# Performance work log

Hardware: AMD Instinct MI355X
Metric: run time of the kernel (lower is better)

The kernel has to match this reference:

```python
import jax, jax.numpy as jnp
import numpy as np

N = 50000
E = 800000
IN_C = 128
HID = 256
OUT_C = 40


def setup_inputs() -> dict:
    key = jax.random.key(0)
    ks = jax.random.split(key, 12)
    def glorot(k, shape):
        lim = float(np.sqrt(6.0 / (shape[0] + shape[1])))
        return jax.random.uniform(k, shape, jnp.float32, -lim, lim)
    x = jax.random.normal(ks[0], (N, IN_C), jnp.float32)
    edge_index = jax.random.randint(ks[1], (2, E), 0, N, jnp.int64)
    edge_weight = jax.random.uniform(ks[2], (E,), jnp.float32)
    return {
        "x": x,
        "edge_index": edge_index,
        "edge_weight": edge_weight,
        "w1_rel": glorot(ks[3], (IN_C, HID)),
        "b1": jnp.zeros((HID,), jnp.float32),
        "w1_root": glorot(ks[4], (IN_C, HID)),
        "w2_rel": glorot(ks[5], (HID, HID)),
        "b2": jnp.zeros((HID,), jnp.float32),
        "w2_root": glorot(ks[6], (HID, HID)),
        "w_lin": glorot(ks[7], (2 * HID, OUT_C)),
        "b_lin": jnp.zeros((OUT_C,), jnp.float32),
    }


def graph_conv(x, src, dst, w, w_rel, b_rel, w_root):
    # PyG GraphConv (aggr='add'): lin_rel(scatter_add(x[src]*w)) + lin_root(x)
    msg = x[src] * w[:, None]                      # [E, F]
    agg = jax.ops.segment_sum(msg, dst, num_segments=N)  # [N, F]
    return agg @ w_rel + b_rel + x @ w_root


def reference(x, edge_index, edge_weight, w1_rel, b1, w1_root,
              w2_rel, b2, w2_root, w_lin, b_lin):
    src, dst = edge_index[0], edge_index[1]
    x1 = jax.nn.relu(graph_conv(x, src, dst, edge_weight, w1_rel, b1, w1_root))
    # dropout is a no-op in eval mode
    x2 = jax.nn.relu(graph_conv(x1, src, dst, edge_weight, w2_rel, b2, w2_root))
    h = jnp.concatenate([x1, x2], axis=-1)         # [N, 2*HID]
    logits = h @ w_lin + b_lin                     # [N, OUT_C]
    return jax.nn.log_softmax(logits, axis=-1)
```

## Files before the change

### kernel.cpp

```cpp
#include <hip/hip_runtime.h>
#include <hip/hip_bf16.h>
#include <hip/hip_fp16.h>
#include <math.h>


typedef __attribute__((ext_vector_type(8))) short short8;
typedef __attribute__((ext_vector_type(4))) float f32x4;

static __device__ __forceinline__ float bf2f(unsigned short u) {
    return __uint_as_float(((unsigned)u) << 16);
}

static __device__ __forceinline__ void fp8x4_to_f32(unsigned u, float* o) {
#if __has_builtin(__builtin_amdgcn_cvt_pk_f32_fp8)
    auto lo = __builtin_amdgcn_cvt_pk_f32_fp8((int)u, false);
    auto hi = __builtin_amdgcn_cvt_pk_f32_fp8((int)u, true);
    o[0] = lo[0]; o[1] = lo[1]; o[2] = hi[0]; o[3] = hi[1];
#else
#pragma unroll
    for (int i = 0; i < 4; ++i) {
        unsigned b = (u >> (8 * i)) & 0xffu;
        unsigned short hb = (unsigned short)(((b & 0x80u) << 8) | ((b & 0x7fu) << 7));
        o[i] = __half2float(__ushort_as_half(hb)) * 256.0f;
    }
#endif
}

static __device__ __forceinline__ unsigned f32_to_fp8(float f) {
    __half h = __float2half(f * 0.00390625f);
    unsigned short hb = __half_as_ushort(h);
    unsigned mag = hb & 0x7fffu;
    unsigned s = (hb >> 8) & 0x80u;
    unsigned v = (mag + 0x3fu + ((mag >> 7) & 1u)) >> 7;
    if (v > 0x7eu) v = 0x7eu;
    return s | v;
}

__global__ __launch_bounds__(256) void scan_block_sums(
    const int* __restrict__ counts, int* __restrict__ bsum, int n)
{
    __shared__ int sh[256];
    int idx = blockIdx.x * 256 + threadIdx.x;
    sh[threadIdx.x] = (idx < n) ? counts[idx] : 0;
    __syncthreads();
#pragma unroll
    for (int off = 128; off; off >>= 1) {
        if (threadIdx.x < off) sh[threadIdx.x] += sh[threadIdx.x + off];
        __syncthreads();
    }
    if (threadIdx.x == 0) bsum[blockIdx.x] = sh[0];
}

__global__ __launch_bounds__(256) void scan_bsum(
    const int* __restrict__ bsum, int* __restrict__ bpre,
    int* __restrict__ bucket_cursor, int nb)
{
    __shared__ int sh[256];
    int t = threadIdx.x;
    int v = (t < nb) ? bsum[t] : 0;
    sh[t] = v;
    __syncthreads();
#pragma unroll
    for (int off = 1; off < 256; off <<= 1) {
        int u = (t >= off) ? sh[t - off] : 0;
        __syncthreads();
        sh[t] += u;
        __syncthreads();
    }
    bpre[t]          = sh[t] - v;
    bucket_cursor[t] = sh[t] - v;
}

__global__ __launch_bounds__(256) void scan_final(
    const int* __restrict__ counts, const int* __restrict__ bpre,
    int* __restrict__ row_ptr, int n, int Etot)
{
    __shared__ int sh[256];
    int t = threadIdx.x;
    int idx = blockIdx.x * 256 + t;
    int v = (idx < n) ? counts[idx] : 0;
    sh[t] = v;
    __syncthreads();
#pragma unroll
    for (int off = 1; off < 256; off <<= 1) {
        int u = (t >= off) ? sh[t - off] : 0;
        __syncthreads();
        sh[t] += u;
        __syncthreads();
    }
    if (idx < n) row_ptr[idx] = bpre[blockIdx.x] + sh[t] - v;
    if (idx == 0) row_ptr[n] = Etot;
}

#define P1_EPB 8
__global__ __launch_bounds__(256) void part_kernel(
    const int* __restrict__ ei, const float* __restrict__ ew,
    int* __restrict__ bucket_cursor, uint2* __restrict__ part, int E)
{
    __shared__ int lhist[256];
    __shared__ int gbase[256];
    const int t = threadIdx.x;
    const int base = blockIdx.x * (256 * P1_EPB);
    lhist[t] = 0;
    __syncthreads();

    int pk[P1_EPB];
#pragma unroll
    for (int i = 0; i < P1_EPB; ++i) {
        int e = base + i * 256 + t;
        if (e < E) {
            int b = ei[E + e] >> 8;
            int r = atomicAdd(&lhist[b], 1);
            pk[i] = (b << 16) | r;
        } else pk[i] = -1;
    }
    __syncthreads();
    if (lhist[t] > 0) gbase[t] = atomicAdd(&bucket_cursor[t], lhist[t]);
    __syncthreads();
#pragma unroll
    for (int i = 0; i < P1_EPB; ++i) {
        if (pk[i] >= 0) {
            int e = base + i * 256 + t;
            int d = ei[E + e];
            unsigned short w16 = __half_as_ushort(__float2half(ew[e]));
            unsigned rec = ((unsigned)w16 << 16) | (unsigned)ei[e];
            int pos = gbase[pk[i] >> 16] + (pk[i] & 0xffff);
            part[pos] = make_uint2(rec, (unsigned)d);
        }
    }
}

__global__ __launch_bounds__(256) void fill2_kernel(
    const uint2* __restrict__ part, const int* __restrict__ bpre,
    const int* __restrict__ bsum, const int* __restrict__ row_ptr,
    unsigned* __restrict__ edges, int n)
{
    __shared__ int curs[256];
    const int b = blockIdx.x;
    const int t = threadIdx.x;
    const int node0 = b << 8;
    if (node0 + t < n) curs[t] = row_ptr[node0 + t];
    __syncthreads();
    const int beg = bpre[b];
    const int end = beg + bsum[b];
    for (int i = beg + t; i < end; i += 256) {
        uint2 p = part[i];
        int slot = atomicAdd(&curs[p.y & 255u], 1);
        edges[slot] = p.x;
    }
}

__global__ __launch_bounds__(256) void prep_all(
    const int* __restrict__ ei, int* __restrict__ counts, int E,
    const float* __restrict__ x, __hip_bfloat16* __restrict__ xb,
    unsigned char* __restrict__ xb8, int NX8,
    const float* __restrict__ w1_rel, const float* __restrict__ w1_root,
    const float* __restrict__ w2_rel, const float* __restrict__ w2_root,
    const float* __restrict__ w_lin,
    __hip_bfloat16* __restrict__ w1relT, __hip_bfloat16* __restrict__ w1rootT,
    __hip_bfloat16* __restrict__ w2relT, __hip_bfloat16* __restrict__ w2rootT,
    __hip_bfloat16* __restrict__ wlinT)
{
    int idx = blockIdx.x * 256 + threadIdx.x;
    if (idx < E) {
        atomicAdd(&counts[ei[E + idx]], 1);
        return;
    }
    idx -= E;
    if (idx < NX8) {
        float4 a = *(const float4*)&x[(size_t)idx * 8];
        float4 b = *(const float4*)&x[(size_t)idx * 8 + 4];
        float f[8] = { a.x, a.y, a.z, a.w, b.x, b.y, b.z, b.w };
        __hip_bfloat16 o[8];
#pragma unroll
        for (int i = 0; i < 8; ++i) o[i] = __float2bfloat16(f[i]);
        *(short8*)&xb[(size_t)idx * 8] = *(short8*)o;
        unsigned p0 = 0, p1 = 0;
#pragma unroll
        for (int i = 0; i < 4; ++i) p0 |= f32_to_fp8(f[i]) << (8 * i);
#pragma unroll
        for (int i = 0; i < 4; ++i) p1 |= f32_to_fp8(f[4 + i]) << (8 * i);
        *(uint2*)&xb8[(size_t)idx * 8] = make_uint2(p0, p1);
        return;
    }
    idx -= NX8;
    if (idx < 65536) {
        const float* src = (idx < 32768) ? w1_rel : w1_root;
        __hip_bfloat16* dst = (idx < 32768) ? w1relT : w1rootT;
        int i = idx & 32767;
        int k = i >> 8, c = i & 255;
        dst[c * 128 + k] = __float2bfloat16(src[i]);
    } else if (idx < 196608) {
        int j = idx - 65536;
        const float* src = (j < 65536) ? w2_rel : w2_root;
        __hip_bfloat16* dst = (j < 65536) ? w2relT : w2rootT;
        int i = j & 65535;
        int k = i >> 8, c = i & 255;
        dst[c * 256 + k] = __float2bfloat16(src[i]);
    } else if (idx < 229376) {
        int i = idx - 196608;
        int seg = i >> 14, c = (i >> 8) & 63, k = i & 255;
        float v = (c < 40) ? w_lin[(size_t)(seg * 256 + k) * 40 + c] : 0.f;
        wlinT[i] = __float2bfloat16(v);
    }
}

template <int C>
__global__ __launch_bounds__(256) void gather_fp8(
    const unsigned char* __restrict__ feat8,
    const unsigned* __restrict__ edges,
    const int*  __restrict__ rp,
    __hip_bfloat16* __restrict__ agg, int n)
{
    const int node = (blockIdx.x * 256 + threadIdx.x) >> 6;
    const int lane = threadIdx.x & 63;
    if (node >= n) return;
    const int beg = __builtin_amdgcn_readfirstlane(rp[node]);
    const int end = __builtin_amdgcn_readfirstlane(rp[node + 1]);

    constexpr int EPW = (C == 128) ? 8 : 4;
    constexpr int LPR = 64 / EPW;
    const int es = lane / LPR;
    const int ch = lane % LPR;
    const unsigned coff = (unsigned)ch * 16;

    float acc[16] = {};

    auto accum16 = [&](uint4 u, float w) {
        unsigned uu[4] = { u.x, u.y, u.z, u.w };
#pragma unroll
        for (int q = 0; q < 4; ++q) {
            float f[4];
            fp8x4_to_f32(uu[q], f);
#pragma unroll
            for (int i = 0; i < 4; ++i)
                acc[q * 4 + i] = fmaf(f[i], w, acc[q * 4 + i]);
        }
    };

    auto unpack_w = [](unsigned p) {
        return __half2float(__ushort_as_half((unsigned short)(p >> 16)));
    };

    for (int base = beg; base < end; base += 64) {
        const int m = min(64, end - base);
        unsigned ev = edges[base + ((lane < m) ? lane : (m - 1))];
        if (lane >= m) ev &= 0xffffu;

        int s = 0;
        for (; s + 2 * EPW <= m; s += 2 * EPW) {
            int j0 = s + es, j1 = j0 + EPW;
            unsigned p0 = (unsigned)__shfl((int)ev, j0, 64);
            unsigned p1 = (unsigned)__shfl((int)ev, j1, 64);
            uint4 u0 = *(const uint4*)(feat8 + (size_t)(p0 & 0xffffu) * C + coff);
            uint4 u1 = *(const uint4*)(feat8 + (size_t)(p1 & 0xffffu) * C + coff);
            accum16(u0, unpack_w(p0));
            accum16(u1, unpack_w(p1));
        }
        for (; s < m; s += EPW) {
            int j = min(s + es, 63);
            unsigned p = (unsigned)__shfl((int)ev, j, 64);
            uint4 u = *(const uint4*)(feat8 + (size_t)(p & 0xffffu) * C + coff);
            accum16(u, unpack_w(p));
        }
    }

#pragma unroll
    for (int k = 0; k < 16; ++k) {
        if constexpr (C == 128) {
            acc[k] += __shfl_xor(acc[k], 8, 64);
            acc[k] += __shfl_xor(acc[k], 16, 64);
            acc[k] += __shfl_xor(acc[k], 32, 64);
        } else {
            acc[k] += __shfl_xor(acc[k], 16, 64);
            acc[k] += __shfl_xor(acc[k], 32, 64);
        }
    }
    if (es == 0) {
        __hip_bfloat16 o[16];
#pragma unroll
        for (int k = 0; k < 16; ++k) o[k] = __float2bfloat16(acc[k]);
        __hip_bfloat16* op = agg + (size_t)node * C + ch * 16;
        *(short8*)op       = *(short8*)o;
        *(short8*)(op + 8) = *(short8*)(o + 8);
    }
}

template <bool WRITE_FP8>
__global__ __launch_bounds__(256) void gemm_mfma(
    const __hip_bfloat16* __restrict__ A0, const __hip_bfloat16* __restrict__ A1,
    const __hip_bfloat16* __restrict__ W0T, const __hip_bfloat16* __restrict__ W1T,
    const float* __restrict__ bias,
    __hip_bfloat16* __restrict__ Cmat,
    unsigned char* __restrict__ Cfp8,
    int n, int K0, int K1)
{
    __shared__ __hip_bfloat16 Asl[2][128 * 64];
    __shared__ __hip_bfloat16 Bsl[2][128 * 64];
    const int bm = blockIdx.x >> 1;
    const int bn = blockIdx.x & 1;
    const int row0 = bm * 128, col0 = bn * 128;
    const int t = threadIdx.x, lane = t & 63, wid = t >> 6;
    const int wr = wid >> 1, wc = wid & 1;

    const int S0 = K0 >> 6;
    const int S  = S0 + (K1 >> 6);

    auto stage = [&](int buf, int s) {
        const __hip_bfloat16* A;
        const __hip_bfloat16* WT;
        int K, k0;
        if (s < S0) { A = A0; WT = W0T; K = K0; k0 = s << 6; }
        else        { A = A1; WT = W1T; K = K1; k0 = (s - S0) << 6; }
#pragma unroll
        for (int i = 0; i < 4; ++i) {
            int idx = i * 256 + t;
            int r = idx >> 3, c = idx & 7;
            int gr = row0 + r; if (gr >= n) gr = n - 1;
            const __hip_bfloat16* srcA =
                A + (size_t)gr * K + k0 + ((c ^ (r & 7)) << 3);
            __builtin_amdgcn_global_load_lds(
                (const __attribute__((address_space(1))) void*)srcA,
                (__attribute__((address_space(3))) void*)&Asl[buf][idx * 8], 16, 0, 0);
            const __hip_bfloat16* srcB =
                WT + (size_t)(col0 + r) * K + k0 + ((c ^ (r & 7)) << 3);
            __builtin_amdgcn_global_load_lds(
                (const __attribute__((address_space(1))) void*)srcB,
                (__attribute__((address_space(3))) void*)&Bsl[buf][idx * 8], 16, 0, 0);
        }
    };

    f32x4 acc[4][4] = {};

    stage(0, 0);
    __syncthreads();

    for (int s = 0; s < S; ++s) {
        const int buf = s & 1;
        if (s + 1 < S) stage(buf ^ 1, s + 1);
#pragma unroll
        for (int kh = 0; kh < 2; ++kh) {
            const int cchunk = kh * 4 + (lane >> 4);
            short8 af[4], bfr[4];
#pragma unroll
            for (int m = 0; m < 4; ++m) {
                int r = wr * 64 + m * 16 + (lane & 15);
                af[m] = *(const short8*)&Asl[buf][r * 64 + ((cchunk ^ (r & 7)) << 3)];
            }
#pragma unroll
            for (int nn = 0; nn < 4; ++nn) {
                int r = wc * 64 + nn * 16 + (lane & 15);
                bfr[nn] = *(const short8*)&Bsl[buf][r * 64 + ((cchunk ^ (r & 7)) << 3)];
            }
#pragma unroll
            for (int m = 0; m < 4; ++m)
#pragma unroll
                for (int nn = 0; nn < 4; ++nn)
                    acc[m][nn] = __builtin_amdgcn_mfma_f32_16x16x32_bf16(
                        af[m], bfr[nn], acc[m][nn], 0, 0, 0);
        }
        __syncthreads();
    }

    __hip_bfloat16* Csh = &Asl[0][0];
#pragma unroll
    for (int nn = 0; nn < 4; ++nn) {
        int lcol = wc * 64 + nn * 16 + (lane & 15);
        float b = bias[col0 + lcol];
#pragma unroll
        for (int m = 0; m < 4; ++m) {
#pragma unroll
            for (int rg = 0; rg < 4; ++rg) {
                int lrow = wr * 64 + m * 16 + ((lane >> 4) * 4) + rg;
                float v = fmaxf(acc[m][nn][rg] + b, 0.f);
                Csh[lrow * 128 + lcol] = __float2bfloat16(v);
            }
        }
    }
    __syncthreads();

#pragma unroll
    for (int it = 0; it < 8; ++it) {
        int idx = it * 256 + t;
        int r = idx >> 4, c16 = idx & 15;
        if (row0 + r < n)
            *(short8*)(Cmat + (size_t)(row0 + r) * 256 + col0 + c16 * 8) =
                *(const short8*)&Csh[r * 128 + c16 * 8];
    }
    if constexpr (WRITE_FP8) {
#pragma unroll
        for (int it = 0; it < 4; ++it) {
            int idx = it * 256 + t;
            int r = idx >> 3, c16 = idx & 7;
            if (row0 + r < n) {
                const __hip_bfloat16* src = &Csh[r * 128 + c16 * 16];
                unsigned w[4];
#pragma unroll
                for (int q = 0; q < 4; ++q) {
                    unsigned p = 0;
#pragma unroll
                    for (int i = 0; i < 4; ++i)
                        p |= f32_to_fp8(__bfloat162float(src[q * 4 + i])) << (8 * i);
                    w[q] = p;
                }
                *(uint4*)(Cfp8 + (size_t)(row0 + r) * 256 + col0 + c16 * 16) =
                    make_uint4(w[0], w[1], w[2], w[3]);
            }
        }
    }
}

__global__ __launch_bounds__(256) void head_mfma(
    const __hip_bfloat16* __restrict__ X1, const __hip_bfloat16* __restrict__ X2,
    const __hip_bfloat16* __restrict__ WLT,
    const float* __restrict__ b_lin,
    float* __restrict__ out, int n)
{
    __shared__ __hip_bfloat16 Asl[128 * 64];
    __shared__ __hip_bfloat16 Bsl[64 * 64];
    const int row0 = blockIdx.x * 128;
    const int t = threadIdx.x, lane = t & 63, wid = t >> 6;

    f32x4 acc[2][4] = {};

    for (int seg = 0; seg < 2; ++seg) {
        const __hip_bfloat16* A  = seg ? X2 : X1;
        const __hip_bfloat16* WT = WLT + seg * 64 * 256;
        for (int k0 = 0; k0 < 256; k0 += 64) {
#pragma unroll
            for (int i = 0; i < 4; ++i) {
                int idx = i * 256 + t;
                int r = idx >> 3, c = idx & 7;
                int gr = row0 + r; if (gr >= n) gr = n - 1;
                const __hip_bfloat16* srcA =
                    A + (size_t)gr * 256 + k0 + ((c ^ (r & 7)) << 3);
                __builtin_amdgcn_global_load_lds(
                    (const __attribute__((address_space(1))) void*)srcA,
                    (__attribute__((address_space(3))) void*)&Asl[idx * 8], 16, 0, 0);
            }
#pragma unroll
            for (int i = 0; i < 2; ++i) {
                int idx = i * 256 + t;
                int r = idx >> 3, c = idx & 7;
                const __hip_bfloat16* srcB =
                    WT + (size_t)r * 256 + k0 + ((c ^ (r & 7)) << 3);
                __builtin_amdgcn_global_load_lds(
                    (const __attribute__((address_space(1))) void*)srcB,
                    (__attribute__((address_space(3))) void*)&Bsl[idx * 8], 16, 0, 0);
            }
            __syncthreads();
#pragma unroll
            for (int kh = 0; kh < 2; ++kh) {
                const int cchunk = kh * 4 + (lane >> 4);
                short8 af[2], bfr[4];
#pragma unroll
                for (int m = 0; m < 2; ++m) {
                    int r = wid * 32 + m * 16 + (lane & 15);
                    af[m] = *(const short8*)&Asl[r * 64 + ((cchunk ^ (r & 7)) << 3)];
                }
#pragma unroll
                for (int nn = 0; nn < 4; ++nn) {
                    int r = nn * 16 + (lane & 15);
                    bfr[nn] = *(const short8*)&Bsl[r * 64 + ((cchunk ^ (r & 7)) << 3)];
                }
#pragma unroll
                for (int m = 0; m < 2; ++m)
#pragma unroll
                    for (int nn = 0; nn < 4; ++nn)
                        acc[m][nn] = __builtin_amdgcn_mfma_f32_16x16x32_bf16(
                            af[m], bfr[nn], acc[m][nn], 0, 0, 0);
            }
            __syncthreads();
        }
    }

    const int cl = lane & 15;
    float bb[4];
#pragma unroll
    for (int nn = 0; nn < 4; ++nn) {
        int col = nn * 16 + cl;
        bb[nn] = (col < 40) ? b_lin[col] : 0.f;
    }
#pragma unroll
    for (int m = 0; m < 2; ++m) {
#pragma unroll
        for (int rg = 0; rg < 4; ++rg) {
            float v[4];
            float mx = -1e30f;
#pragma unroll
            for (int nn = 0; nn < 4; ++nn) {
                int col = nn * 16 + cl;
                v[nn] = acc[m][nn][rg] + bb[nn];
                if (col < 40) mx = fmaxf(mx, v[nn]);
            }
#pragma unroll
            for (int off = 1; off < 16; off <<= 1)
                mx = fmaxf(mx, __shfl_xor(mx, off, 64));
            float s = 0.f;
#pragma unroll
            for (int nn = 0; nn < 4; ++nn) {
                int col = nn * 16 + cl;
                if (col < 40) s += expf(v[nn] - mx);
            }
#pragma unroll
            for (int off = 1; off < 16; off <<= 1)
                s += __shfl_xor(s, off, 64);
            float ls = logf(s);
            int row = row0 + wid * 32 + m * 16 + ((lane >> 4) * 4) + rg;
            if (row < n) {
#pragma unroll
                for (int nn = 0; nn < 4; ++nn) {
                    int col = nn * 16 + cl;
                    if (col < 40)
                        out[(size_t)row * 40 + col] = v[nn] - mx - ls;
                }
            }
        }
    }
}

extern "C" void kernel_launch(void* const* d_in, const int* in_sizes, int n_in,
                              void* d_out, int out_size, void* d_ws, size_t ws_size,
                              hipStream_t stream)
{
    const float* x       = (const float*)d_in[0];
    const int*   ei      = (const int*)  d_in[1];
    const float* ew      = (const float*)d_in[2];
    const float* w1_rel  = (const float*)d_in[3];
    const float* b1      = (const float*)d_in[4];
    const float* w1_root = (const float*)d_in[5];
    const float* w2_rel  = (const float*)d_in[6];
    const float* b2      = (const float*)d_in[7];
    const float* w2_root = (const float*)d_in[8];
    const float* w_lin   = (const float*)d_in[9];
    const float* b_lin   = (const float*)d_in[10];
    float* out = (float*)d_out;

    const int N = in_sizes[0] / 128;
    const int E = in_sizes[2];

    auto align = [](char*& p, size_t bytes) {
        char* r = p;
        p += (bytes + 255) & ~(size_t)255;
        return r;
    };
    char* wp = (char*)d_ws;
    __hip_bfloat16* xb     = (__hip_bfloat16*)align(wp, (size_t)N * 128 * 2);
    __hip_bfloat16* agg1b  = (__hip_bfloat16*)align(wp, (size_t)N * 128 * 2);
    __hip_bfloat16* x1b    = (__hip_bfloat16*)align(wp, (size_t)N * 256 * 2);
    __hip_bfloat16* agg2b  = (__hip_bfloat16*)align(wp, (size_t)N * 256 * 2);
    __hip_bfloat16* x2b    = (__hip_bfloat16*)align(wp, (size_t)N * 256 * 2);
    unsigned char*  xb8    = (unsigned char*)align(wp, (size_t)N * 128);
    unsigned char*  x1b8   = (unsigned char*)align(wp, (size_t)N * 256);
    __hip_bfloat16* w1relT  = (__hip_bfloat16*)align(wp, 256 * 128 * 2);
    __hip_bfloat16* w1rootT = (__hip_bfloat16*)align(wp, 256 * 128 * 2);
    __hip_bfloat16* w2relT  = (__hip_bfloat16*)align(wp, 256 * 256 * 2);
    __hip_bfloat16* w2rootT = (__hip_bfloat16*)align(wp, 256 * 256 * 2);
    __hip_bfloat16* wlinT   = (__hip_bfloat16*)align(wp, 2 * 64 * 256 * 2);
    int*      counts        = (int*)align(wp, (size_t)N * 4);
    int*      row_ptr       = (int*)align(wp, (size_t)(N + 1) * 4);
    int*      bsum          = (int*)align(wp, 256 * 4);
    int*      bpre          = (int*)align(wp, 256 * 4);
    int*      bucket_cursor = (int*)align(wp, 256 * 4);
    unsigned* edges         = (unsigned*)align(wp, (size_t)E * 4);
    uint2*    part          = (uint2*)align(wp, (size_t)E * 8);

    const int eb = (E + 255) / 256;
    const int nb = (N + 255) / 256;

    hipMemsetAsync(counts, 0, (size_t)N * 4, stream);
    const int NX8 = N * 128 / 8;
    {
        long long total = (long long)E + NX8 + 229376;
        int blocks = (int)((total + 255) / 256);
        prep_all<<<blocks, 256, 0, stream>>>(
            ei, counts, E, x, xb, xb8, NX8,
            w1_rel, w1_root, w2_rel, w2_root, w_lin,
            w1relT, w1rootT, w2relT, w2rootT, wlinT);
    }
    scan_block_sums<<<nb, 256, 0, stream>>>(counts, bsum, N);
    scan_bsum<<<1, 256, 0, stream>>>(bsum, bpre, bucket_cursor, nb);
    scan_final<<<nb, 256, 0, stream>>>(counts, bpre, row_ptr, N, E);
    {
        int p1_blocks = (E + 256 * P1_EPB - 1) / (256 * P1_EPB);
        part_kernel<<<p1_blocks, 256, 0, stream>>>(ei, ew, bucket_cursor, part, E);
        fill2_kernel<<<nb, 256, 0, stream>>>(part, bpre, bsum, row_ptr, edges, N);
    }

    const int gather_blocks = (N * 64 + 255) / 256;
    const int gemm_grid     = ((N + 127) / 128) * 2;
    const int head_grid     = (N + 127) / 128;

    gather_fp8<128><<<gather_blocks, 256, 0, stream>>>(
        xb8, edges, row_ptr, agg1b, N);
    gemm_mfma<true><<<gemm_grid, 256, 0, stream>>>(
        agg1b, xb, w1relT, w1rootT, b1, x1b, x1b8, N, 128, 128);
    gather_fp8<256><<<gather_blocks, 256, 0, stream>>>(
        x1b8, edges, row_ptr, agg2b, N);
    gemm_mfma<false><<<gemm_grid, 256, 0, stream>>>(
        agg2b, x1b, w2relT, w2rootT, b2, x2b, nullptr, N, 256, 256);
    head_mfma<<<head_grid, 256, 0, stream>>>(x1b, x2b, wlinT, b_lin, out, N);
}
```

Before: 208.0 us.

## Replace per-node count and scans with bucket histogram and in-fill local scan

Removes the per-node global atomic degree counting, the block-sum scan and the final scan. Instead, a shared-memory bucket histogram over 256-node buckets is built, and fill2_kernel computes per-node counts and an exclusive scan locally from the partitioned edges, writing row_ptr itself. This cuts global atomics and two kernel launches, but fill2 now reads the partitioned edges twice.

Result: faster. 181.8 us (-12.6%).

```diff
diff --git a/kernel.cpp b/kernel.cpp
--- a/kernel.cpp
+++ b/kernel.cpp
@@ -36,28 +36,31 @@
     return s | v;
 }
 
-__global__ __launch_bounds__(256) void scan_block_sums(
-    const int* __restrict__ counts, int* __restrict__ bsum, int n)
-{
-    __shared__ int sh[256];
-    int idx = blockIdx.x * 256 + threadIdx.x;
-    sh[threadIdx.x] = (idx < n) ? counts[idx] : 0;
-    __syncthreads();
-#pragma unroll
-    for (int off = 128; off; off >>= 1) {
-        if (threadIdx.x < off) sh[threadIdx.x] += sh[threadIdx.x + off];
-        __syncthreads();
-    }
-    if (threadIdx.x == 0) bsum[blockIdx.x] = sh[0];
+#define BH_EPB 16
+__global__ __launch_bounds__(256) void bucket_hist(
+    const int* __restrict__ ei, int* __restrict__ bhist, int E)
+{
+    __shared__ int lh[256];
+    const int t = threadIdx.x;
+    lh[t] = 0;
+    __syncthreads();
+    const int base = blockIdx.x * (256 * BH_EPB);
+#pragma unroll
+    for (int i = 0; i < BH_EPB; ++i) {
+        int e = base + i * 256 + t;
+        if (e < E) atomicAdd(&lh[ei[E + e] >> 8], 1);
+    }
+    __syncthreads();
+    if (lh[t] > 0) atomicAdd(&bhist[t], lh[t]);
 }
 
 __global__ __launch_bounds__(256) void scan_bsum(
-    const int* __restrict__ bsum, int* __restrict__ bpre,
+    const int* __restrict__ bhist, int* __restrict__ bpre,
     int* __restrict__ bucket_cursor, int nb)
 {
     __shared__ int sh[256];
     int t = threadIdx.x;
-    int v = (t < nb) ? bsum[t] : 0;
+    int v = (t < nb) ? bhist[t] : 0;
     sh[t] = v;
     __syncthreads();
 #pragma unroll
@@ -69,27 +72,6 @@
     }
     bpre[t]          = sh[t] - v;
     bucket_cursor[t] = sh[t] - v;
-}
-
-__global__ __launch_bounds__(256) void scan_final(
-    const int* __restrict__ counts, const int* __restrict__ bpre,
-    int* __restrict__ row_ptr, int n, int Etot)
-{
-    __shared__ int sh[256];
-    int t = threadIdx.x;
-    int idx = blockIdx.x * 256 + t;
-    int v = (idx < n) ? counts[idx] : 0;
-    sh[t] = v;
-    __syncthreads();
-#pragma unroll
-    for (int off = 1; off < 256; off <<= 1) {
-        int u = (t >= off) ? sh[t - off] : 0;
-        __syncthreads();
-        sh[t] += u;
-        __syncthreads();
-    }
-    if (idx < n) row_ptr[idx] = bpre[blockIdx.x] + sh[t] - v;
-    if (idx == 0) row_ptr[n] = Etot;
 }
 
 #define P1_EPB 8
@@ -132,17 +114,37 @@
 
 __global__ __launch_bounds__(256) void fill2_kernel(
     const uint2* __restrict__ part, const int* __restrict__ bpre,
-    const int* __restrict__ bsum, const int* __restrict__ row_ptr,
+    const int* __restrict__ bhist, int* __restrict__ row_ptr,
     unsigned* __restrict__ edges, int n)
 {
+    __shared__ int lcnt[256];
+    __shared__ int excl[256];
     __shared__ int curs[256];
     const int b = blockIdx.x;
     const int t = threadIdx.x;
     const int node0 = b << 8;
-    if (node0 + t < n) curs[t] = row_ptr[node0 + t];
+    lcnt[t] = 0;
     __syncthreads();
     const int beg = bpre[b];
-    const int end = beg + bsum[b];
+    const int end = beg + bhist[b];
+    for (int i = beg + t; i < end; i += 256)
+        atomicAdd(&lcnt[part[i].y & 255u], 1);
+    __syncthreads();
+    int v = lcnt[t];
+    excl[t] = v;
+    __syncthreads();
+#pragma unroll
+    for (int off = 1; off < 256; off <<= 1) {
+        int u = (t >= off) ? excl[t - off] : 0;
+        __syncthreads();
+        excl[t] += u;
+        __syncthreads();
+    }
+    const int base_t = beg + excl[t] - v;
+    const int nd = node0 + t;
+    if (nd <= n) row_ptr[nd] = base_t;
+    curs[t] = base_t;
+    __syncthreads();
     for (int i = beg + t; i < end; i += 256) {
         uint2 p = part[i];
         int slot = atomicAdd(&curs[p.y & 255u], 1);
@@ -151,7 +153,6 @@
 }
 
 __global__ __launch_bounds__(256) void prep_all(
-    const int* __restrict__ ei, int* __restrict__ counts, int E,
     const float* __restrict__ x, __hip_bfloat16* __restrict__ xb,
     unsigned char* __restrict__ xb8, int NX8,
     const float* __restrict__ w1_rel, const float* __restrict__ w1_root,
@@ -162,11 +163,6 @@
     __hip_bfloat16* __restrict__ wlinT)
 {
     int idx = blockIdx.x * 256 + threadIdx.x;
-    if (idx < E) {
-        atomicAdd(&counts[ei[E + idx]], 1);
-        return;
-    }
-    idx -= E;
     if (idx < NX8) {
         float4 a = *(const float4*)&x[(size_t)idx * 8];
         float4 b = *(const float4*)&x[(size_t)idx * 8 + 4];
@@ -557,34 +553,32 @@
     __hip_bfloat16* w2relT  = (__hip_bfloat16*)align(wp, 256 * 256 * 2);
     __hip_bfloat16* w2rootT = (__hip_bfloat16*)align(wp, 256 * 256 * 2);
     __hip_bfloat16* wlinT   = (__hip_bfloat16*)align(wp, 2 * 64 * 256 * 2);
-    int*      counts        = (int*)align(wp, (size_t)N * 4);
     int*      row_ptr       = (int*)align(wp, (size_t)(N + 1) * 4);
-    int*      bsum          = (int*)align(wp, 256 * 4);
+    int*      bhist         = (int*)align(wp, 256 * 4);
     int*      bpre          = (int*)align(wp, 256 * 4);
     int*      bucket_cursor = (int*)align(wp, 256 * 4);
     unsigned* edges         = (unsigned*)align(wp, (size_t)E * 4);
     uint2*    part          = (uint2*)align(wp, (size_t)E * 8);
 
-    const int eb = (E + 255) / 256;
     const int nb = (N + 255) / 256;
 
-    hipMemsetAsync(counts, 0, (size_t)N * 4, stream);
+    hipMemsetAsync(bhist, 0, 256 * 4, stream);
     const int NX8 = N * 128 / 8;
     {
-        long long total = (long long)E + NX8 + 229376;
+        long long total = (long long)NX8 + 229376;
         int blocks = (int)((total + 255) / 256);
         prep_all<<<blocks, 256, 0, stream>>>(
-            ei, counts, E, x, xb, xb8, NX8,
+            x, xb, xb8, NX8,
             w1_rel, w1_root, w2_rel, w2_root, w_lin,
             w1relT, w1rootT, w2relT, w2rootT, wlinT);
     }
-    scan_block_sums<<<nb, 256, 0, stream>>>(counts, bsum, N);
-    scan_bsum<<<1, 256, 0, stream>>>(bsum, bpre, bucket_cursor, nb);
-    scan_final<<<nb, 256, 0, stream>>>(counts, bpre, row_ptr, N, E);
     {
+        int bh_blocks = (E + 256 * BH_EPB - 1) / (256 * BH_EPB);
+        bucket_hist<<<bh_blocks, 256, 0, stream>>>(ei, bhist, E);
+        scan_bsum<<<1, 256, 0, stream>>>(bhist, bpre, bucket_cursor, nb);
         int p1_blocks = (E + 256 * P1_EPB - 1) / (256 * P1_EPB);
         part_kernel<<<p1_blocks, 256, 0, stream>>>(ei, ew, bucket_cursor, part, E);
-        fill2_kernel<<<nb, 256, 0, stream>>>(part, bpre, bsum, row_ptr, edges, N);
+        fill2_kernel<<<nb, 256, 0, stream>>>(part, bpre, bhist, row_ptr, edges, N);
     }
 
     const int gather_blocks = (N * 64 + 255) / 256;
```
